# Performance work log

Measured on AMD Instinct MI355X. Metric: run time of the kernel, lower is better.

Reference implementation:

```python
import jax, jax.numpy as jnp
import numpy as np
import math

L, Bt, IN, H = 512, 128, 512, 60


def setup_inputs() -> dict:
    key = jax.random.key(0)
    k1, k2, k3 = jax.random.split(key, 3)
    inp = jax.random.normal(k1, (L, Bt, IN), dtype=jnp.float32)
    W = jax.random.normal(k2, (H, IN), dtype=jnp.float32) / np.sqrt(IN)
    b = jnp.zeros((H,), dtype=jnp.float32)
    alphabet = jax.random.uniform(k3, (H, 3), dtype=jnp.float32, minval=-math.pi, maxval=math.pi)
    bond_lengths = jnp.array([132.868, 145.801, 152.326], dtype=jnp.float32)
    bond_angles = jnp.array([2.028, 2.124, 1.941], dtype=jnp.float32)
    return {"inp": inp, "W": W, "b": b, "alphabet": alphabet,
            "bond_lengths": bond_lengths, "bond_angles": bond_angles}


def reference(inp, W, b, alphabet, bond_lengths, bond_angles):
    Lr, Bb = inp.shape[0], inp.shape[1]
    # mixture over alphabet of torsion angles
    x = jax.nn.softmax(inp @ W.T + b, axis=2)                 # (L, B, H)
    phi = jnp.arctan2(x @ jnp.sin(alphabet), x @ jnp.cos(alphabet))  # (L, B, 3)
    # per residue i the loop consumes phi[i].T -> bond index is fastest axis
    phi_f = phi.transpose(0, 2, 1).reshape(Lr * 3, Bb)        # (3L, B)
    r = jnp.tile(bond_lengths, Lr)[:, None]                   # (3L, 1)
    th = jnp.tile(bond_angles, Lr)[:, None]                   # (3L, 1)
    # SRF coordinates of every new atom
    c_tilde = jnp.stack([
        (r * jnp.cos(th)) * jnp.ones_like(phi_f),
        r * jnp.cos(phi_f) * jnp.sin(th),
        r * jnp.sin(phi_f) * jnp.sin(th),
    ], axis=-1)                                               # (3L, B, 3)

    e = jnp.eye(3, dtype=inp.dtype)
    carry0 = (jnp.broadcast_to(e[0], (Bb, 3)),
              jnp.broadcast_to(e[1], (Bb, 3)),
              jnp.broadcast_to(e[2], (Bb, 3)))

    def step(carry, ct):
        A, Bp, C = carry                                      # each (B, 3)
        BC = C - Bp
        bc = BC / jnp.linalg.norm(BC, axis=1, keepdims=True)
        AB = Bp - A
        Nv = jnp.cross(AB, bc)
        n = Nv / jnp.linalg.norm(Nv, axis=1, keepdims=True)
        # D = C + R @ c_tilde, R columns = [bc, n x bc, n]
        D = C + bc * ct[:, 0:1] + jnp.cross(n, bc) * ct[:, 1:2] + n * ct[:, 2:3]
        return (Bp, C, D), D

    _, coords = jax.lax.scan(step, carry0, c_tilde)           # (3L, B, 3)
    return coords
```

## Files before the change

kernel.cpp:

```cpp
#include <hip/hip_runtime.h>
#include <math.h>

#define LSEQ  512
#define BT    128
#define INF   512
#define HH    60
#define NSTEP 1536
#define CHUNK 24

#define MTILE 128
#define BROW  264

typedef __attribute__((ext_vector_type(8))) short bf16x8;
typedef __attribute__((ext_vector_type(4))) float floatx4;

__device__ __forceinline__ unsigned short bf16_rn(float x) {
  unsigned u = __float_as_uint(x);
  return (unsigned short)((u + 0x7FFFu + ((u >> 16) & 1u)) >> 16);
}
__device__ __forceinline__ void split2(float x, unsigned short& h, unsigned short& l) {
  h = bf16_rn(x);
  float hf = __uint_as_float(((unsigned)h) << 16);
  l = bf16_rn(x - hf);
}

__global__ __launch_bounds__(256) void k_wconv(
    const float* __restrict__ W, unsigned short* __restrict__ Wh,
    unsigned short* __restrict__ Wl) {
  const int idx = blockIdx.x * 256 + threadIdx.x;
  const int h = idx >> 9, k = idx & 511;
  float x = (h < HH) ? W[h * INF + k] : 0.f;
  unsigned short hb, lb; split2(x, hb, lb);
  Wh[idx] = hb; Wl[idx] = lb;
}

__global__ __launch_bounds__(256, 2) void k_phi(
    const float* __restrict__ inp, const unsigned short* __restrict__ Wh,
    const unsigned short* __restrict__ Wl, const float* __restrict__ bias,
    const float* __restrict__ alphabet, float* __restrict__ phi_out) {
  __shared__ unsigned short BhL[64 * BROW];
  __shared__ unsigned short BlL[64 * BROW];
  __shared__ float sS[HH * 3], sC[HH * 3], sBias[64];

  const int tid  = threadIdx.x;
  const int lane = tid & 63;
  const int wid  = tid >> 6;
  const int c    = lane & 15;
  const int quad = lane >> 4;
  const int row0 = blockIdx.x * MTILE;

  if (tid < HH * 3) { float a = alphabet[tid]; sS[tid] = __sinf(a); sC[tid] = __cosf(a); }
  if (tid >= 192 && tid < 256) { int n = tid - 192; sBias[n] = (n < HH) ? bias[n] : 0.f; }

  floatx4 acc[2][4];
#pragma unroll
  for (int mt = 0; mt < 2; ++mt)
#pragma unroll
    for (int nt = 0; nt < 4; ++nt) acc[mt][nt] = (floatx4){0.f, 0.f, 0.f, 0.f};

  const float* ap0 = inp + (size_t)(row0 + wid * 32 + c)      * INF + quad * 8;
  const float* ap1 = ap0 + 16 * INF;

  for (int half = 0; half < 2; ++half) {
    const int kbase = half * 256;
    if (half) __syncthreads();
#pragma unroll
    for (int i = 0; i < 8; ++i) {
      const int chunk = i * 256 + tid;
      const int r = chunk >> 5;
      const int j = (chunk & 31) * 8;
      *(uint4*)&BhL[r * BROW + j] = *(const uint4*)(Wh + (size_t)r * INF + kbase + j);
      *(uint4*)&BlL[r * BROW + j] = *(const uint4*)(Wl + (size_t)r * INF + kbase + j);
    }
    __syncthreads();

    float4 pa0, pa1, pa2, pa3;
    pa0 = *(const float4*)(ap0 + kbase);
    pa1 = *(const float4*)(ap0 + kbase + 4);
    pa2 = *(const float4*)(ap1 + kbase);
    pa3 = *(const float4*)(ap1 + kbase + 4);

#pragma unroll
    for (int ks = 0; ks < 8; ++ks) {
      const int kl = ks * 32;
      float4 a00 = pa0, a01 = pa1, a10 = pa2, a11 = pa3;
      if (ks + 1 < 8) {
        pa0 = *(const float4*)(ap0 + kbase + kl + 32);
        pa1 = *(const float4*)(ap0 + kbase + kl + 36);
        pa2 = *(const float4*)(ap1 + kbase + kl + 32);
        pa3 = *(const float4*)(ap1 + kbase + kl + 36);
      }
      bf16x8 Bh[4], Bl[4];
#pragma unroll
      for (int nt = 0; nt < 4; ++nt) {
        const int boff = (nt * 16 + c) * BROW + kl + quad * 8;
        Bh[nt] = *(const bf16x8*)&BhL[boff];
        Bl[nt] = *(const bf16x8*)&BlL[boff];
      }
      bf16x8 Ah[2], Al[2];
      {
        float av[2][8] = {{a00.x,a00.y,a00.z,a00.w,a01.x,a01.y,a01.z,a01.w},
                          {a10.x,a10.y,a10.z,a10.w,a11.x,a11.y,a11.z,a11.w}};
#pragma unroll
        for (int mt = 0; mt < 2; ++mt)
#pragma unroll
          for (int j = 0; j < 8; ++j) {
            unsigned short hb, lb; split2(av[mt][j], hb, lb);
            Ah[mt][j] = (short)hb; Al[mt][j] = (short)lb;
          }
      }
#pragma unroll
      for (int mt = 0; mt < 2; ++mt)
#pragma unroll
        for (int nt = 0; nt < 4; ++nt) {
          acc[mt][nt] = __builtin_amdgcn_mfma_f32_16x16x32_bf16(Ah[mt], Bh[nt], acc[mt][nt], 0, 0, 0);
          acc[mt][nt] = __builtin_amdgcn_mfma_f32_16x16x32_bf16(Ah[mt], Bl[nt], acc[mt][nt], 0, 0, 0);
          acc[mt][nt] = __builtin_amdgcn_mfma_f32_16x16x32_bf16(Al[mt], Bh[nt], acc[mt][nt], 0, 0, 0);
        }
    }
  }

#pragma unroll
  for (int mt = 0; mt < 2; ++mt) {
#pragma unroll
    for (int reg = 0; reg < 4; ++reg) {
      float lg[4];  bool val[4];
#pragma unroll
      for (int nt = 0; nt < 4; ++nt) {
        const int n = nt * 16 + c;
        val[nt] = (n < HH);
        lg[nt] = acc[mt][nt][reg] + sBias[n];
      }
      float m = -1e30f;
#pragma unroll
      for (int nt = 0; nt < 4; ++nt) if (val[nt]) m = fmaxf(m, lg[nt]);
#pragma unroll
      for (int d = 1; d < 16; d <<= 1) m = fmaxf(m, __shfl_xor(m, d, 64));

      float s0=0.f,c0=0.f,s1=0.f,c1=0.f,s2=0.f,c2=0.f;
#pragma unroll
      for (int nt = 0; nt < 4; ++nt) {
        const int n = nt * 16 + c;
        float e = val[nt] ? __expf(lg[nt] - m) : 0.f;
        s0 = fmaf(e, sS[n*3+0], s0);  c0 = fmaf(e, sC[n*3+0], c0);
        s1 = fmaf(e, sS[n*3+1], s1);  c1 = fmaf(e, sC[n*3+1], c1);
        s2 = fmaf(e, sS[n*3+2], s2);  c2 = fmaf(e, sC[n*3+2], c2);
      }
#pragma unroll
      for (int d = 1; d < 16; d <<= 1) {
        s0 += __shfl_xor(s0, d, 64);  c0 += __shfl_xor(c0, d, 64);
        s1 += __shfl_xor(s1, d, 64);  c1 += __shfl_xor(c1, d, 64);
        s2 += __shfl_xor(s2, d, 64);  c2 += __shfl_xor(c2, d, 64);
      }
      if (c == 0) {
        const int row = row0 + wid * 32 + mt * 16 + quad * 4 + reg;
        const int l  = row >> 7;
        const int bb = row & 127;
        float* pp = phi_out + (size_t)bb * NSTEP + 3 * l;
        pp[0] = atan2f(s0, c0);
        pp[1] = atan2f(s1, c1);
        pp[2] = atan2f(s2, c2);
      }
    }
  }
}

struct Xf { float r[9]; float p[3]; };

__device__ __forceinline__ Xf compose(const Xf& A, const Xf& B) {
  Xf o;
#pragma unroll
  for (int i = 0; i < 3; ++i) {
#pragma unroll
    for (int j = 0; j < 3; ++j) {
      o.r[i*3+j] = fmaf(A.r[i*3+0], B.r[0+j],
                   fmaf(A.r[i*3+1], B.r[3+j],
                        A.r[i*3+2] * B.r[6+j]));
    }
    o.p[i] = fmaf(A.r[i*3+0], B.p[0],
             fmaf(A.r[i*3+1], B.p[1],
             fmaf(A.r[i*3+2], B.p[2], A.p[i])));
  }
  return o;
}

__device__ __forceinline__ Xf make_T(float phi, float st, float ct, float r) {
  float sp = __sinf(phi), cp = __cosf(phi);
  Xf T;
  T.r[0] = ct;      T.r[1] = -st;     T.r[2] = 0.f;
  T.r[3] = cp * st; T.r[4] = ct * cp; T.r[5] = -sp;
  T.r[6] = sp * st; T.r[7] = ct * sp; T.r[8] = cp;
  T.p[0] = r * ct;  T.p[1] = r * T.r[3]; T.p[2] = r * T.r[6];
  return T;
}

__device__ __forceinline__ void set_identity(Xf& X) {
  X.r[0]=1.f; X.r[1]=0.f; X.r[2]=0.f;
  X.r[3]=0.f; X.r[4]=1.f; X.r[5]=0.f;
  X.r[6]=0.f; X.r[7]=0.f; X.r[8]=1.f;
  X.p[0]=0.f; X.p[1]=0.f; X.p[2]=0.f;
}

__global__ __launch_bounds__(64) void k_scan(
    const float* __restrict__ phi, const float* __restrict__ bl,
    const float* __restrict__ ba, float* __restrict__ out) {
  const int b = blockIdx.x;
  const int t = threadIdx.x;

  float st[3], ct[3], rr[3];
#pragma unroll
  for (int j = 0; j < 3; ++j) {
    float a = ba[j];
    st[j] = __sinf(a); ct[j] = __cosf(a); rr[j] = bl[j];
  }

  float f[CHUNK];
  const float4* ph4 = (const float4*)(phi + (size_t)b * NSTEP + t * CHUNK);
#pragma unroll
  for (int q = 0; q < CHUNK/4; ++q) {
    float4 v = ph4[q];
    f[4*q+0] = v.x; f[4*q+1] = v.y; f[4*q+2] = v.z; f[4*q+3] = v.w;
  }

  Xf Q = make_T(f[0], st[0], ct[0], rr[0]);
#pragma unroll
  for (int s = 1; s < CHUNK; ++s)
    Q = compose(Q, make_T(f[s], st[s%3], ct[s%3], rr[s%3]));

#pragma unroll
  for (int d = 1; d < 64; d <<= 1) {
    Xf O;
#pragma unroll
    for (int q = 0; q < 9; ++q) O.r[q] = __shfl_up(Q.r[q], d, 64);
#pragma unroll
    for (int q = 0; q < 3; ++q) O.p[q] = __shfl_up(Q.p[q], d, 64);
    if (t < d) set_identity(O);
    Q = compose(O, Q);
  }

  Xf E;
#pragma unroll
  for (int q = 0; q < 9; ++q) E.r[q] = __shfl_up(Q.r[q], 1, 64);
#pragma unroll
  for (int q = 0; q < 3; ++q) E.p[q] = __shfl_up(Q.p[q], 1, 64);
  if (t == 0) set_identity(E);

  Xf S0;
  S0.r[0] = 0.f;                  S0.r[1] = 0.816496580927726f;   S0.r[2] = 0.5773502691896258f;
  S0.r[3] = -0.7071067811865475f; S0.r[4] = -0.4082482904638631f; S0.r[5] = 0.5773502691896258f;
  S0.r[6] = 0.7071067811865475f;  S0.r[7] = -0.4082482904638631f; S0.r[8] = 0.5773502691896258f;
  S0.p[0] = 0.f; S0.p[1] = 0.f; S0.p[2] = 1.f;

  Xf cur = compose(S0, E);

  float* op = out + (size_t)(t * CHUNK) * (BT * 3) + b * 3;
#pragma unroll
  for (int s = 0; s < CHUNK; ++s) {
    cur = compose(cur, make_T(f[s], st[s%3], ct[s%3], rr[s%3]));
    op[(size_t)s * (BT*3) + 0] = cur.p[0];
    op[(size_t)s * (BT*3) + 1] = cur.p[1];
    op[(size_t)s * (BT*3) + 2] = cur.p[2];
  }
}

extern "C" void kernel_launch(void* const* d_in, const int* in_sizes, int n_in,
                              void* d_out, int out_size, void* d_ws, size_t ws_size,
                              hipStream_t stream) {
  const float* inp      = (const float*)d_in[0];
  const float* W        = (const float*)d_in[1];
  const float* bias     = (const float*)d_in[2];
  const float* alphabet = (const float*)d_in[3];
  const float* bl       = (const float*)d_in[4];
  const float* ba       = (const float*)d_in[5];
  float* out = (float*)d_out;

  float* phi = (float*)d_ws;
  unsigned short* Wh = (unsigned short*)((char*)d_ws + 786432);
  unsigned short* Wl = Wh + 64 * INF;

  k_wconv<<<dim3(128), dim3(256), 0, stream>>>(W, Wh, Wl);
  k_phi<<<dim3((LSEQ*BT)/MTILE), dim3(256), 0, stream>>>(inp, Wh, Wl, bias, alphabet, phi);
  k_scan<<<dim3(BT), dim3(64), 0, stream>>>(phi, bl, ba, out);
}
```

Baseline: 220.5 us.

## Fuse W bf16 split into GEMM kernel and widen scan to four waves

Removes the separate W-conversion kernel launch: each k_phi block now loads fp32 W directly and splits it into bf16 hi/lo while filling shared memory. The scan kernel goes from 64 threads with 24 steps each to 256 threads with 6 steps each. It adds a cross-wave prefix through shared memory, so the serial per-thread compose chain is shorter. The cost is redundant W conversion in every GEMM block, plus an extra barrier and up to three composes per thread in the scan.

Result: no change. 222.0 us (+0.7%).

```diff
diff --git a/kernel.cpp b/kernel.cpp
--- a/kernel.cpp
+++ b/kernel.cpp
@@ -6,13 +6,14 @@
 #define INF   512
 #define HH    60
 #define NSTEP 1536
-#define CHUNK 24
+#define CH2   6
 
 #define MTILE 128
 #define BROW  264
 
 typedef __attribute__((ext_vector_type(8))) short bf16x8;
 typedef __attribute__((ext_vector_type(4))) float floatx4;
+typedef __attribute__((ext_vector_type(4))) unsigned short ushortx4;
 
 __device__ __forceinline__ unsigned short bf16_rn(float x) {
   unsigned u = __float_as_uint(x);
@@ -24,20 +25,10 @@
   l = bf16_rn(x - hf);
 }
 
-__global__ __launch_bounds__(256) void k_wconv(
-    const float* __restrict__ W, unsigned short* __restrict__ Wh,
-    unsigned short* __restrict__ Wl) {
-  const int idx = blockIdx.x * 256 + threadIdx.x;
-  const int h = idx >> 9, k = idx & 511;
-  float x = (h < HH) ? W[h * INF + k] : 0.f;
-  unsigned short hb, lb; split2(x, hb, lb);
-  Wh[idx] = hb; Wl[idx] = lb;
-}
-
 __global__ __launch_bounds__(256, 2) void k_phi(
-    const float* __restrict__ inp, const unsigned short* __restrict__ Wh,
-    const unsigned short* __restrict__ Wl, const float* __restrict__ bias,
-    const float* __restrict__ alphabet, float* __restrict__ phi_out) {
+    const float* __restrict__ inp, const float* __restrict__ W,
+    const float* __restrict__ bias, const float* __restrict__ alphabet,
+    float* __restrict__ phi_out) {
   __shared__ unsigned short BhL[64 * BROW];
   __shared__ unsigned short BlL[64 * BROW];
   __shared__ float sS[HH * 3], sC[HH * 3], sBias[64];
@@ -65,12 +56,20 @@
     const int kbase = half * 256;
     if (half) __syncthreads();
 #pragma unroll
-    for (int i = 0; i < 8; ++i) {
+    for (int i = 0; i < 16; ++i) {
       const int chunk = i * 256 + tid;
-      const int r = chunk >> 5;
-      const int j = (chunk & 31) * 8;
-      *(uint4*)&BhL[r * BROW + j] = *(const uint4*)(Wh + (size_t)r * INF + kbase + j);
-      *(uint4*)&BlL[r * BROW + j] = *(const uint4*)(Wl + (size_t)r * INF + kbase + j);
+      const int r  = chunk >> 6;
+      const int j4 = (chunk & 63) * 4;
+      float4 wv = make_float4(0.f, 0.f, 0.f, 0.f);
+      if (r < HH) wv = *(const float4*)(W + (size_t)r * INF + kbase + j4);
+      ushortx4 hv, lv;
+      unsigned short hb, lb;
+      split2(wv.x, hb, lb); hv[0] = hb; lv[0] = lb;
+      split2(wv.y, hb, lb); hv[1] = hb; lv[1] = lb;
+      split2(wv.z, hb, lb); hv[2] = hb; lv[2] = lb;
+      split2(wv.w, hb, lb); hv[3] = hb; lv[3] = lb;
+      *(ushortx4*)&BhL[r * BROW + j4] = hv;
+      *(ushortx4*)&BlL[r * BROW + j4] = lv;
     }
     __syncthreads();
 
@@ -201,11 +200,15 @@
   X.p[0]=0.f; X.p[1]=0.f; X.p[2]=0.f;
 }
 
-__global__ __launch_bounds__(64) void k_scan(
+__global__ __launch_bounds__(256) void k_scan(
     const float* __restrict__ phi, const float* __restrict__ bl,
     const float* __restrict__ ba, float* __restrict__ out) {
+  __shared__ Xf wt[4];
+
   const int b = blockIdx.x;
-  const int t = threadIdx.x;
+  const int t = threadIdx.x & 63;
+  const int w = threadIdx.x >> 6;
+  const int g = threadIdx.x;
 
   float st[3], ct[3], rr[3];
 #pragma unroll
@@ -214,17 +217,17 @@
     st[j] = __sinf(a); ct[j] = __cosf(a); rr[j] = bl[j];
   }
 
-  float f[CHUNK];
-  const float4* ph4 = (const float4*)(phi + (size_t)b * NSTEP + t * CHUNK);
-#pragma unroll
-  for (int q = 0; q < CHUNK/4; ++q) {
-    float4 v = ph4[q];
-    f[4*q+0] = v.x; f[4*q+1] = v.y; f[4*q+2] = v.z; f[4*q+3] = v.w;
+  float f[CH2];
+  const float2* ph2 = (const float2*)(phi + (size_t)b * NSTEP + g * CH2);
+#pragma unroll
+  for (int q = 0; q < CH2/2; ++q) {
+    float2 v = ph2[q];
+    f[2*q+0] = v.x; f[2*q+1] = v.y;
   }
 
   Xf Q = make_T(f[0], st[0], ct[0], rr[0]);
 #pragma unroll
-  for (int s = 1; s < CHUNK; ++s)
+  for (int s = 1; s < CH2; ++s)
     Q = compose(Q, make_T(f[s], st[s%3], ct[s%3], rr[s%3]));
 
 #pragma unroll
@@ -237,6 +240,9 @@
     if (t < d) set_identity(O);
     Q = compose(O, Q);
   }
+
+  if (t == 63) wt[w] = Q;
+  __syncthreads();
 
   Xf E;
 #pragma unroll
@@ -251,11 +257,16 @@
   S0.r[6] = 0.7071067811865475f;  S0.r[7] = -0.4082482904638631f; S0.r[8] = 0.5773502691896258f;
   S0.p[0] = 0.f; S0.p[1] = 0.f; S0.p[2] = 1.f;
 
-  Xf cur = compose(S0, E);
-
-  float* op = out + (size_t)(t * CHUNK) * (BT * 3) + b * 3;
-#pragma unroll
-  for (int s = 0; s < CHUNK; ++s) {
+  Xf SP = S0;
+#pragma unroll
+  for (int i = 0; i < 3; ++i)
+    if (i < w) SP = compose(SP, wt[i]);
+
+  Xf cur = compose(SP, E);
+
+  float* op = out + (size_t)(g * CH2) * (BT * 3) + b * 3;
+#pragma unroll
+  for (int s = 0; s < CH2; ++s) {
     cur = compose(cur, make_T(f[s], st[s%3], ct[s%3], rr[s%3]));
     op[(size_t)s * (BT*3) + 0] = cur.p[0];
     op[(size_t)s * (BT*3) + 1] = cur.p[1];
@@ -275,10 +286,7 @@
   float* out = (float*)d_out;
 
   float* phi = (float*)d_ws;
-  unsigned short* Wh = (unsigned short*)((char*)d_ws + 786432);
-  unsigned short* Wl = Wh + 64 * INF;
-
-  k_wconv<<<dim3(128), dim3(256), 0, stream>>>(W, Wh, Wl);
-  k_phi<<<dim3((LSEQ*BT)/MTILE), dim3(256), 0, stream>>>(inp, Wh, Wl, bias, alphabet, phi);
-  k_scan<<<dim3(BT), dim3(64), 0, stream>>>(phi, bl, ba, out);
-}
+
+  k_phi<<<dim3((LSEQ*BT)/MTILE), dim3(256), 0, stream>>>(inp, W, bias, alphabet, phi);
+  k_scan<<<dim3(BT), dim3(256), 0, stream>>>(phi, bl, ba, out);
+}
```
